# Optimization experiments

Measured on AMD Instinct MI355X. Metric: run time of the kernel, lower is better.

## Reference

```python
import jax, jax.numpy as jnp
import numpy as np

SCALE = 8.0  # sqrt(d_k=64)


def setup_inputs() -> dict:
    key = jax.random.key(0)
    kq, kk, kv, km = jax.random.split(key, 4)
    B, L, D = 8, 4096, 64
    q = jax.random.normal(kq, (B, L, D), dtype=jnp.float32)
    k = jax.random.normal(kk, (B, L, D), dtype=jnp.float32)
    v = jax.random.normal(kv, (B, L, D), dtype=jnp.float32)
    mask = jax.random.randint(km, (B, L, L), 0, 2) == 1  # True = masked out
    return {"q": q, "k": k, "v": v, "mask": mask}


def reference(q, k, v, mask):
    # scores: [B, Lq, Lk]
    u = jnp.einsum('bqd,bkd->bqk', q, k) / SCALE
    u = jnp.where(mask, -jnp.inf, u)
    attn = jax.nn.softmax(u, axis=2)
    output = jnp.einsum('bqk,bkd->bqd', attn, v)
    return (attn, output)
```

## Files before the change

kernel.cpp:

```cpp
#include <hip/hip_runtime.h>
#include <hip/hip_bf16.h>
#include <stdint.h>

#define BB 8
#define LL 4096
#define DD 64
#define KT 64
#define NT (LL / KT)
#define NP2 (LL / 128)

typedef short bf16x8 __attribute__((ext_vector_type(8)));
typedef short bf16x2 __attribute__((ext_vector_type(2)));
typedef float f32x4 __attribute__((ext_vector_type(4)));

#define QSCALE 0.1803368801111204f

__device__ inline short f2bfs(float x) {
    __hip_bfloat16 h = __float2bfloat16(x);
    return __builtin_bit_cast(short, h);
}

__device__ inline bf16x8 pack8v(f32x4 a, f32x4 b) {
    bf16x8 r;
    r[0] = f2bfs(a[0]); r[1] = f2bfs(a[1]); r[2] = f2bfs(a[2]); r[3] = f2bfs(a[3]);
    r[4] = f2bfs(b[0]); r[5] = f2bfs(b[1]); r[6] = f2bfs(b[2]); r[7] = f2bfs(b[3]);
    return r;
}

__device__ inline int swzK(int r) { return (r & 3) | (((r >> 3) & 1) << 2); }
__device__ inline int swzV(int r) { return (r & 7) ^ ((r >> 3) & 7); }

__device__ inline void wg_barrier() {
    asm volatile("s_waitcnt lgkmcnt(0)" ::: "memory");
    __builtin_amdgcn_s_barrier();
    __builtin_amdgcn_sched_barrier(0);
}

__global__ void detect_mask_kernel(const uint32_t* __restrict__ w, uint32_t* __restrict__ flag) {
    __shared__ int nonbin;
    if (threadIdx.x == 0) nonbin = 0;
    __syncthreads();
    int bad = 0;
    for (int i = threadIdx.x; i < 4096; i += 256) bad |= (w[i] > 1u) ? 1 : 0;
    if (bad) atomicOr(&nonbin, 1);
    __syncthreads();
    if (threadIdx.x == 0) *flag = (uint32_t)(nonbin != 0);
}

__global__ __launch_bounds__(512, 4) void fused_attn_kernel(
    const float* __restrict__ qg, const float* __restrict__ kg,
    const float* __restrict__ vg, const void* __restrict__ maskv,
    const uint32_t* __restrict__ flagp,
    float* __restrict__ attn, float* __restrict__ outp)
{
    __shared__ alignas(16) ushort KB[4][KT * 64];
    __shared__ uint8_t Msk[8][NT][64];
    __shared__ float Rs[128];

    const int tid = (int)threadIdx.x;
    const int w   = tid >> 6, l = tid & 63;
    const int lr  = l & 15, lg = l >> 4;
    const int rg  = w & 3, ch = w >> 2;
    const int id  = (int)blockIdx.x;
    const int b   = id & 7;
    const int q0  = (id >> 3) * 64;
    const bool mbyte = (*flagp != 0);

    const float* kb = kg + (size_t)b * LL * DD;
    const float* vb = vg + (size_t)b * LL * DD;

    const int qrow = q0 + 16 * rg + lr;
    const uint8_t* mrow8  = (const uint8_t*)maskv + (size_t)b * LL * LL + (size_t)qrow * LL + ch * 32 + lg * 8;
    const int*     mrow32 = (const int*)maskv     + (size_t)b * LL * LL + (size_t)qrow * LL + ch * 32 + lg * 8;
    float* arow = attn + (size_t)b * LL * LL + (size_t)qrow * LL + ch * 32 + lg * 8;

    bf16x8 qf0, qf1;
    {
        const float* qp = qg + (size_t)(b * LL + qrow) * DD + lg * 8;
        qf0 = pack8v(*(const f32x4*)(qp)      * QSCALE, *(const f32x4*)(qp + 4)  * QSCALE);
        qf1 = pack8v(*(const f32x4*)(qp + 32) * QSCALE, *(const f32x4*)(qp + 36) * QSCALE);
    }

    const int krow0 = tid >> 3, kc8 = tid & 7;
    const int vk2 = tid >> 4, vd4 = tid & 15;

    f32x4 kS0, kS1, vS0, vS1; uint64_t mS = 0;
    auto issS = [&](int kt) {
        const int kbase = kt * KT;
        const float* p = kb + (size_t)(kbase + krow0) * DD + kc8 * 8;
        kS0 = *(const f32x4*)p; kS1 = *(const f32x4*)(p + 4);
        const float* pv = vb + (size_t)(kbase + vk2 * 2) * DD + vd4 * 4;
        vS0 = *(const f32x4*)pv; vS1 = *(const f32x4*)(pv + DD);
        if (mbyte) mS = *(const uint64_t*)(mrow8 + kbase);
    };
    auto comS = [&](int buf) {
        *(bf16x8*)&KB[buf][krow0 * 64 + ((kc8 ^ swzK(krow0)) << 3)] = pack8v(kS0, kS1);
        const int k0 = vk2 * 2;
        #pragma unroll
        for (int e = 0; e < 4; ++e) {
            const int d = vd4 * 4 + e;
            bf16x2 t; t[0] = f2bfs(vS0[e]); t[1] = f2bfs(vS1[e]);
            *(bf16x2*)&KB[2 + buf][d * 64 + (((k0 >> 3) ^ swzV(d)) << 3) + (k0 & 7)] = t;
        }
    };

    float rsum = 0.f;
    f32x4 oacc[4];
    #pragma unroll
    for (int g = 0; g < 4; ++g) { f32x4 z = {0.f, 0.f, 0.f, 0.f}; oacc[g] = z; }

    auto p1body = [&](int buf, uint64_t mu, int kt) {
        const int kbase = kt * KT;
        int4 mi0 = {0,0,0,0}, mi1 = {0,0,0,0};
        if (!mbyte) { mi0 = *(const int4*)(mrow32 + kbase); mi1 = *(const int4*)(mrow32 + kbase + 4); }
        uint32_t mbits = 0;
        float p8[8];
        #pragma unroll
        for (int n = 0; n < 2; ++n) {
            const int krow = ch * 32 + ((lr >> 2) << 3) + (n << 2) + (lr & 3);
            bf16x8 k0 = *(const bf16x8*)&KB[buf][krow * 64 + ((lg       ^ swzK(krow)) << 3)];
            bf16x8 k1 = *(const bf16x8*)&KB[buf][krow * 64 + (((4 + lg) ^ swzK(krow)) << 3)];
            f32x4 c = {0.f, 0.f, 0.f, 0.f};
            c = __builtin_amdgcn_mfma_f32_16x16x32_bf16(k0, qf0, c, 0, 0, 0);
            c = __builtin_amdgcn_mfma_f32_16x16x32_bf16(k1, qf1, c, 0, 0, 0);
            #pragma unroll
            for (int j = 0; j < 4; ++j) {
                const int t = n * 4 + j;
                int mk;
                if (mbyte) mk = (int)((mu >> (8 * t)) & 0xffu);
                else {
                    const int4 mi = n ? mi1 : mi0;
                    mk = (j == 0) ? mi.x : (j == 1) ? mi.y : (j == 2) ? mi.z : mi.w;
                }
                mbits |= (mk ? 1u : 0u) << t;
                const float pv = mk ? 0.f : exp2f(c[j]);
                rsum += pv;
                p8[t] = pv;
            }
        }
        Msk[w][kt][l] = (uint8_t)mbits;
        bf16x8 pa;
        #pragma unroll
        for (int t = 0; t < 8; ++t) pa[t] = f2bfs(p8[t]);
        __builtin_amdgcn_s_setprio(1);
        #pragma unroll
        for (int g = 0; g < 4; ++g) {
            const int d = g * 16 + lr;
            bf16x8 vf = *(const bf16x8*)&KB[2 + buf][d * 64 + (((ch * 4 + lg) ^ swzV(d)) << 3)];
            oacc[g] = __builtin_amdgcn_mfma_f32_16x16x32_bf16(pa, vf, oacc[g], 0, 0, 0);
        }
        __builtin_amdgcn_s_setprio(0);
    };

    issS(0);
    __builtin_amdgcn_sched_barrier(0);
    comS(0);
    wg_barrier();
    #pragma unroll 1
    for (int kt = 0; kt < NT; ++kt) {
        const int cur = kt & 1;
        const bool more = (kt < NT - 1);
        const uint64_t mu = mS;
        if (more) issS(kt + 1);
        __builtin_amdgcn_sched_barrier(0);
        p1body(cur, mu, kt);
        if (more) comS(cur ^ 1);
        wg_barrier();
    }

    rsum += __shfl_xor(rsum, 16, 64);
    rsum += __shfl_xor(rsum, 32, 64);
    if (lg == 0) Rs[ch * 64 + 16 * rg + lr] = rsum;
    __syncthreads();
    const float rinv = 1.0f / (Rs[16 * rg + lr] + Rs[64 + 16 * rg + lr]);

    float* OutL = (float*)KB;
    if (ch == 1) {
        #pragma unroll
        for (int g = 0; g < 4; ++g)
            #pragma unroll
            for (int j = 0; j < 4; ++j)
                OutL[rg * 1088 + (lg * 4 + j) * 68 + g * 16 + lr] = oacc[g][j];
    }
    __syncthreads();
    if (ch == 0) {
        #pragma unroll
        for (int j = 0; j < 4; ++j) {
            const int ql = 16 * rg + lg * 4 + j;
            const float ri = 1.0f / (Rs[ql] + Rs[64 + ql]);
            const size_t orow = (size_t)(b * LL + q0 + ql) * DD;
            #pragma unroll
            for (int g = 0; g < 4; ++g)
                outp[orow + g * 16 + lr] = (oacc[g][j] + OutL[rg * 1088 + (lg * 4 + j) * 68 + g * 16 + lr]) * ri;
        }
    }
    __syncthreads();

    f32x4 k2[4];
    auto iss2 = [&](int kt2) {
        #pragma unroll
        for (int m = 0; m < 2; ++m) {
            const float* p = kb + (size_t)(kt2 * 128 + krow0 + 64 * m) * DD + kc8 * 8;
            k2[2 * m]     = *(const f32x4*)p;
            k2[2 * m + 1] = *(const f32x4*)(p + 4);
        }
    };
    auto com2 = [&](int pair) {
        #pragma unroll
        for (int m = 0; m < 2; ++m)
            *(bf16x8*)&KB[2 * pair + m][krow0 * 64 + ((kc8 ^ swzK(krow0)) << 3)] = pack8v(k2[2 * m], k2[2 * m + 1]);
    };
    auto p2body = [&](int pair, int idx) {
        const int kbase2 = idx * 128;
        #pragma unroll
        for (int h = 0; h < 2; ++h) {
            const int mb2 = (int)Msk[w][2 * idx + h][l];
            const ushort* Kbuf = KB[2 * pair + h];
            #pragma unroll
            for (int n = 0; n < 2; ++n) {
                const int krow = ch * 32 + ((lr >> 2) << 3) + (n << 2) + (lr & 3);
                bf16x8 k0 = *(const bf16x8*)&Kbuf[krow * 64 + ((lg       ^ swzK(krow)) << 3)];
                bf16x8 k1 = *(const bf16x8*)&Kbuf[krow * 64 + (((4 + lg) ^ swzK(krow)) << 3)];
                f32x4 c = {0.f, 0.f, 0.f, 0.f};
                c = __builtin_amdgcn_mfma_f32_16x16x32_bf16(k0, qf0, c, 0, 0, 0);
                c = __builtin_amdgcn_mfma_f32_16x16x32_bf16(k1, qf1, c, 0, 0, 0);
                f32x4 pv;
                #pragma unroll
                for (int j = 0; j < 4; ++j)
                    pv[j] = ((mb2 >> (n * 4 + j)) & 1) ? 0.f : exp2f(c[j]) * rinv;
                *(f32x4*)(arow + kbase2 + h * 64 + n * 4) = pv;
            }
        }
    };

    iss2(0);
    __builtin_amdgcn_sched_barrier(0);
    com2(0);
    wg_barrier();
    #pragma unroll 1
    for (int kt2 = 0; kt2 < NP2; ++kt2) {
        const int pair = kt2 & 1;
        const bool more = (kt2 < NP2 - 1);
        if (more) iss2(kt2 + 1);
        __builtin_amdgcn_sched_barrier(0);
        p2body(pair, kt2);
        if (more) com2(pair ^ 1);
        wg_barrier();
    }
}

extern "C" void kernel_launch(void* const* d_in, const int* in_sizes, int n_in,
                              void* d_out, int out_size, void* d_ws, size_t ws_size,
                              hipStream_t stream) {
    const float* q = (const float*)d_in[0];
    const float* k = (const float*)d_in[1];
    const float* v = (const float*)d_in[2];
    const void* mask = d_in[3];
    float* attn = (float*)d_out;
    float* outp = attn + (size_t)BB * LL * LL;
    uint32_t* flagp = (uint32_t*)d_ws;

    detect_mask_kernel<<<1, 256, 0, stream>>>((const uint32_t*)mask, flagp);
    fused_attn_kernel<<<dim3((LL / 64) * BB), 512, 0, stream>>>(q, k, v, mask, flagp, attn, outp);
}
```

Before: 368.1 us.

## Deepen phase-1 K/V prefetch to two tiles ahead and drop loop-tail branches

Phase 1 now keeps two register staging sets (A/B) and issues global loads for tile kt+2 while computing tile kt. This gives more time to hide memory latency. The loop is unrolled by two and wraps indices modulo the tile count, so the last iterations do redundant but harmless loads and LDS writes instead of branching. Phase 2 likewise drops the 'more' guard and always prefetches with a wrapped index. The cost is more live registers and some wasted loads and stores at the tail.

Result: no change. 362.7 us (-1.5%).

```diff
diff --git a/kernel.cpp b/kernel.cpp
--- a/kernel.cpp
+++ b/kernel.cpp
@@ -84,22 +84,41 @@
     const int krow0 = tid >> 3, kc8 = tid & 7;
     const int vk2 = tid >> 4, vd4 = tid & 15;
 
-    f32x4 kS0, kS1, vS0, vS1; uint64_t mS = 0;
-    auto issS = [&](int kt) {
+    f32x4 kA0, kA1, vA0, vA1; uint64_t mA = 0;
+    f32x4 kB0, kB1, vB0, vB1; uint64_t mB = 0;
+    auto issA = [&](int kt) {
         const int kbase = kt * KT;
         const float* p = kb + (size_t)(kbase + krow0) * DD + kc8 * 8;
-        kS0 = *(const f32x4*)p; kS1 = *(const f32x4*)(p + 4);
+        kA0 = *(const f32x4*)p; kA1 = *(const f32x4*)(p + 4);
         const float* pv = vb + (size_t)(kbase + vk2 * 2) * DD + vd4 * 4;
-        vS0 = *(const f32x4*)pv; vS1 = *(const f32x4*)(pv + DD);
-        if (mbyte) mS = *(const uint64_t*)(mrow8 + kbase);
-    };
-    auto comS = [&](int buf) {
-        *(bf16x8*)&KB[buf][krow0 * 64 + ((kc8 ^ swzK(krow0)) << 3)] = pack8v(kS0, kS1);
+        vA0 = *(const f32x4*)pv; vA1 = *(const f32x4*)(pv + DD);
+        if (mbyte) mA = *(const uint64_t*)(mrow8 + kbase);
+    };
+    auto issB = [&](int kt) {
+        const int kbase = kt * KT;
+        const float* p = kb + (size_t)(kbase + krow0) * DD + kc8 * 8;
+        kB0 = *(const f32x4*)p; kB1 = *(const f32x4*)(p + 4);
+        const float* pv = vb + (size_t)(kbase + vk2 * 2) * DD + vd4 * 4;
+        vB0 = *(const f32x4*)pv; vB1 = *(const f32x4*)(pv + DD);
+        if (mbyte) mB = *(const uint64_t*)(mrow8 + kbase);
+    };
+    auto comA = [&](int buf) {
+        *(bf16x8*)&KB[buf][krow0 * 64 + ((kc8 ^ swzK(krow0)) << 3)] = pack8v(kA0, kA1);
         const int k0 = vk2 * 2;
         #pragma unroll
         for (int e = 0; e < 4; ++e) {
             const int d = vd4 * 4 + e;
-            bf16x2 t; t[0] = f2bfs(vS0[e]); t[1] = f2bfs(vS1[e]);
+            bf16x2 t; t[0] = f2bfs(vA0[e]); t[1] = f2bfs(vA1[e]);
+            *(bf16x2*)&KB[2 + buf][d * 64 + (((k0 >> 3) ^ swzV(d)) << 3) + (k0 & 7)] = t;
+        }
+    };
+    auto comB = [&](int buf) {
+        *(bf16x8*)&KB[buf][krow0 * 64 + ((kc8 ^ swzK(krow0)) << 3)] = pack8v(kB0, kB1);
+        const int k0 = vk2 * 2;
+        #pragma unroll
+        for (int e = 0; e < 4; ++e) {
+            const int d = vd4 * 4 + e;
+            bf16x2 t; t[0] = f2bfs(vB0[e]); t[1] = f2bfs(vB1[e]);
             *(bf16x2*)&KB[2 + buf][d * 64 + (((k0 >> 3) ^ swzV(d)) << 3) + (k0 & 7)] = t;
         }
     };
@@ -152,20 +171,28 @@
         __builtin_amdgcn_s_setprio(0);
     };
 
-    issS(0);
+    issA(0); issB(1);
     __builtin_amdgcn_sched_barrier(0);
-    comS(0);
+    comA(0);
     wg_barrier();
     #pragma unroll 1
-    for (int kt = 0; kt < NT; ++kt) {
-        const int cur = kt & 1;
-        const bool more = (kt < NT - 1);
-        const uint64_t mu = mS;
-        if (more) issS(kt + 1);
-        __builtin_amdgcn_sched_barrier(0);
-        p1body(cur, mu, kt);
-        if (more) comS(cur ^ 1);
-        wg_barrier();
+    for (int kt = 0; kt < NT; kt += 2) {
+        {
+            const uint64_t mu = mA;
+            issA((kt + 2) & (NT - 1));
+            __builtin_amdgcn_sched_barrier(0);
+            p1body(0, mu, kt);
+            comB(1);
+            wg_barrier();
+        }
+        {
+            const uint64_t mu = mB;
+            issB((kt + 3) & (NT - 1));
+            __builtin_amdgcn_sched_barrier(0);
+            p1body(1, mu, kt + 1);
+            comA(0);
+            wg_barrier();
+        }
     }
 
     rsum += __shfl_xor(rsum, 16, 64);
@@ -240,11 +267,10 @@
     #pragma unroll 1
     for (int kt2 = 0; kt2 < NP2; ++kt2) {
         const int pair = kt2 & 1;
-        const bool more = (kt2 < NP2 - 1);
-        if (more) iss2(kt2 + 1);
+        iss2((kt2 + 1) & (NP2 - 1));
         __builtin_amdgcn_sched_barrier(0);
         p2body(pair, kt2);
-        if (more) com2(pair ^ 1);
+        com2(pair ^ 1);
         wg_barrier();
     }
 }
```

## Pre-convert K and transposed V to bf16 and stream tiles via direct-to-LDS loads

Applied to the files above, without the earlier changes.

Adds two prep kernels: one converts K to bf16, the other converts V to a transposed bf16 layout, both written into workspace. The main kernel then fills its swizzled LDS tiles with global_load_lds DMA instead of register loads followed by convert-and-store. Both phases get a two-deep prefetch pipeline controlled by explicit vmcnt waits. This halves the bytes of K/V read per block and removes the VALU conversion work from the hot loop, at the cost of extra launches and hand-tuned waitcnt accounting. Phase 2 also adds int32-mask loads whose results are never used.

New measurement: 352.6 us. 4.2% less time.

```diff
diff --git a/kernel.cpp b/kernel.cpp
--- a/kernel.cpp
+++ b/kernel.cpp
@@ -10,7 +10,6 @@
 #define NP2 (LL / 128)
 
 typedef short bf16x8 __attribute__((ext_vector_type(8)));
-typedef short bf16x2 __attribute__((ext_vector_type(2)));
 typedef float f32x4 __attribute__((ext_vector_type(4)));
 
 #define QSCALE 0.1803368801111204f
@@ -36,6 +35,11 @@
     __builtin_amdgcn_sched_barrier(0);
 }
 
+__device__ inline void gl_lds16(const ushort* g, ushort* l) {
+    __builtin_amdgcn_global_load_lds((const __attribute__((address_space(1))) void*)g,
+                                     (__attribute__((address_space(3))) void*)l, 16, 0, 0);
+}
+
 __global__ void detect_mask_kernel(const uint32_t* __restrict__ w, uint32_t* __restrict__ flag) {
     __shared__ int nonbin;
     if (threadIdx.x == 0) nonbin = 0;
@@ -47,9 +51,36 @@
     if (threadIdx.x == 0) *flag = (uint32_t)(nonbin != 0);
 }
 
+__global__ void convert_k_kernel(const float* __restrict__ src, ushort* __restrict__ dst) {
+    const int i = blockIdx.x * 256 + threadIdx.x;
+    f32x4 a = *(const f32x4*)(src + (size_t)i * 8);
+    f32x4 b = *(const f32x4*)(src + (size_t)i * 8 + 4);
+    *(bf16x8*)(dst + (size_t)i * 8) = pack8v(a, b);
+}
+
+__global__ void convert_vt_kernel(const float* __restrict__ v, ushort* __restrict__ vt) {
+    __shared__ alignas(16) float Lt[64][68];
+    const int kt = blockIdx.x, b = blockIdx.y;
+    const int tid = (int)threadIdx.x;
+    const int r = tid >> 2, c4 = tid & 3;
+    const float* vb = v + ((size_t)b * LL + kt * 64) * DD;
+    #pragma unroll
+    for (int j = 0; j < 4; ++j)
+        *(f32x4*)&Lt[r][c4 * 16 + j * 4] = *(const f32x4*)(vb + (size_t)r * DD + c4 * 16 + j * 4);
+    __syncthreads();
+    ushort* vout = vt + (size_t)b * DD * LL + (size_t)r * LL + kt * 64 + c4 * 16;
+    bf16x8 o0, o1;
+    #pragma unroll
+    for (int j = 0; j < 8; ++j) o0[j] = f2bfs(Lt[c4 * 16 + j][r]);
+    #pragma unroll
+    for (int j = 0; j < 8; ++j) o1[j] = f2bfs(Lt[c4 * 16 + 8 + j][r]);
+    *(bf16x8*)vout = o0;
+    *(bf16x8*)(vout + 8) = o1;
+}
+
 __global__ __launch_bounds__(512, 4) void fused_attn_kernel(
-    const float* __restrict__ qg, const float* __restrict__ kg,
-    const float* __restrict__ vg, const void* __restrict__ maskv,
+    const float* __restrict__ qg, const ushort* __restrict__ kbf,
+    const ushort* __restrict__ vtb, const void* __restrict__ maskv,
     const uint32_t* __restrict__ flagp,
     float* __restrict__ attn, float* __restrict__ outp)
 {
@@ -66,8 +97,8 @@
     const int q0  = (id >> 3) * 64;
     const bool mbyte = (*flagp != 0);
 
-    const float* kb = kg + (size_t)b * LL * DD;
-    const float* vb = vg + (size_t)b * LL * DD;
+    const ushort* kb = kbf + (size_t)b * LL * DD;
+    const ushort* vtg = vtb + (size_t)b * DD * LL;
 
     const int qrow = q0 + 16 * rg + lr;
     const uint8_t* mrow8  = (const uint8_t*)maskv + (size_t)b * LL * LL + (size_t)qrow * LL + ch * 32 + lg * 8;
@@ -81,38 +112,33 @@
         qf1 = pack8v(*(const f32x4*)(qp + 32) * QSCALE, *(const f32x4*)(qp + 36) * QSCALE);
     }
 
-    const int krow0 = tid >> 3, kc8 = tid & 7;
-    const int vk2 = tid >> 4, vd4 = tid & 15;
-
-    f32x4 kS0, kS1, vS0, vS1; uint64_t mS = 0;
-    auto issS = [&](int kt) {
-        const int kbase = kt * KT;
-        const float* p = kb + (size_t)(kbase + krow0) * DD + kc8 * 8;
-        kS0 = *(const f32x4*)p; kS1 = *(const f32x4*)(p + 4);
-        const float* pv = vb + (size_t)(kbase + vk2 * 2) * DD + vd4 * 4;
-        vS0 = *(const f32x4*)pv; vS1 = *(const f32x4*)(pv + DD);
-        if (mbyte) mS = *(const uint64_t*)(mrow8 + kbase);
-    };
-    auto comS = [&](int buf) {
-        *(bf16x8*)&KB[buf][krow0 * 64 + ((kc8 ^ swzK(krow0)) << 3)] = pack8v(kS0, kS1);
-        const int k0 = vk2 * 2;
-        #pragma unroll
-        for (int e = 0; e < 4; ++e) {
-            const int d = vd4 * 4 + e;
-            bf16x2 t; t[0] = f2bfs(vS0[e]); t[1] = f2bfs(vS1[e]);
-            *(bf16x2*)&KB[2 + buf][d * 64 + (((k0 >> 3) ^ swzV(d)) << 3) + (k0 & 7)] = t;
-        }
-    };
+    const int drow = w * 8 + (l >> 3);
+    const int dc   = l & 7;
+    const int kchunk = dc ^ swzK(drow);
+    const int vchunk = dc ^ swzV(drow);
+    ushort* ldsK0 = &KB[0][0] + (tid >> 6) * 512;
+    auto dmaK = [&](int kt, int buf) {
+        gl_lds16(kb + (size_t)(kt * KT + drow) * 64 + 8 * kchunk, &KB[buf][w * 512]);
+    };
+    auto dmaV = [&](int kt, int buf) {
+        gl_lds16(vtg + (size_t)drow * LL + kt * KT + 8 * vchunk, &KB[2 + buf][w * 512]);
+    };
+    auto dmaK2 = [&](int kt2, int pair) {
+        gl_lds16(kb + (size_t)(kt2 * 128 + drow) * 64 + 8 * kchunk, &KB[2 * pair][w * 512]);
+        gl_lds16(kb + (size_t)(kt2 * 128 + 64 + drow) * 64 + 8 * kchunk, &KB[2 * pair + 1][w * 512]);
+    };
+    unsigned long long mA = 0, mB = 0;
+    #define ASM_MLOAD(dst, kt) { unsigned long long a_ = (unsigned long long)(uintptr_t)(mrow8 + (kt) * KT); \
+        asm volatile("global_load_dwordx2 %0, %1, off" : "=v"(dst) : "v"(a_) : "memory"); }
 
     float rsum = 0.f;
     f32x4 oacc[4];
     #pragma unroll
     for (int g = 0; g < 4; ++g) { f32x4 z = {0.f, 0.f, 0.f, 0.f}; oacc[g] = z; }
 
-    auto p1body = [&](int buf, uint64_t mu, int kt) {
-        const int kbase = kt * KT;
+    auto body1 = [&](int buf, unsigned long long mu, int kt) {
         int4 mi0 = {0,0,0,0}, mi1 = {0,0,0,0};
-        if (!mbyte) { mi0 = *(const int4*)(mrow32 + kbase); mi1 = *(const int4*)(mrow32 + kbase + 4); }
+        if (!mbyte) { mi0 = *(const int4*)(mrow32 + kt * KT); mi1 = *(const int4*)(mrow32 + kt * KT + 4); }
         uint32_t mbits = 0;
         float p8[8];
         #pragma unroll
@@ -152,20 +178,24 @@
         __builtin_amdgcn_s_setprio(0);
     };
 
-    issS(0);
-    __builtin_amdgcn_sched_barrier(0);
-    comS(0);
-    wg_barrier();
+    dmaK(0, 0); dmaV(0, 0); if (mbyte) ASM_MLOAD(mA, 0);
+    dmaK(1, 1); dmaV(1, 1); if (mbyte) ASM_MLOAD(mB, 1);
     #pragma unroll 1
-    for (int kt = 0; kt < NT; ++kt) {
-        const int cur = kt & 1;
-        const bool more = (kt < NT - 1);
-        const uint64_t mu = mS;
-        if (more) issS(kt + 1);
+    for (int kt = 0; kt < NT; kt += 2) {
+        if (mbyte) asm volatile("s_waitcnt vmcnt(3)" ::: "memory");
+        else       asm volatile("s_waitcnt vmcnt(2)" ::: "memory");
         __builtin_amdgcn_sched_barrier(0);
-        p1body(cur, mu, kt);
-        if (more) comS(cur ^ 1);
-        wg_barrier();
+        wg_barrier();
+        body1(0, mA, kt);
+        wg_barrier();
+        if (kt + 2 < NT) { dmaK(kt + 2, 0); dmaV(kt + 2, 0); if (mbyte) ASM_MLOAD(mA, kt + 2); }
+        if (mbyte) asm volatile("s_waitcnt vmcnt(3)" ::: "memory");
+        else       asm volatile("s_waitcnt vmcnt(2)" ::: "memory");
+        __builtin_amdgcn_sched_barrier(0);
+        wg_barrier();
+        body1(1, mB, kt + 1);
+        wg_barrier();
+        if (kt + 3 < NT) { dmaK(kt + 3, 1); dmaV(kt + 3, 1); if (mbyte) ASM_MLOAD(mB, kt + 3); }
     }
 
     rsum += __shfl_xor(rsum, 16, 64);
@@ -196,26 +226,18 @@
     }
     __syncthreads();
 
-    f32x4 k2[4];
-    auto iss2 = [&](int kt2) {
-        #pragma unroll
-        for (int m = 0; m < 2; ++m) {
-            const float* p = kb + (size_t)(kt2 * 128 + krow0 + 64 * m) * DD + kc8 * 8;
-            k2[2 * m]     = *(const f32x4*)p;
-            k2[2 * m + 1] = *(const f32x4*)(p + 4);
-        }
-    };
-    auto com2 = [&](int pair) {
-        #pragma unroll
-        for (int m = 0; m < 2; ++m)
-            *(bf16x8*)&KB[2 * pair + m][krow0 * 64 + ((kc8 ^ swzK(krow0)) << 3)] = pack8v(k2[2 * m], k2[2 * m + 1]);
-    };
-    auto p2body = [&](int pair, int idx) {
+    auto body2 = [&](int pair, int idx) {
         const int kbase2 = idx * 128;
         #pragma unroll
         for (int h = 0; h < 2; ++h) {
             const int mb2 = (int)Msk[w][2 * idx + h][l];
             const ushort* Kbuf = KB[2 * pair + h];
+            int4 mi0 = {0,0,0,0}, mi1 = {0,0,0,0};
+            if (!mbyte) {
+                mi0 = *(const int4*)(mrow32 + kbase2 + h * 64);
+                mi1 = *(const int4*)(mrow32 + kbase2 + h * 64 + 4);
+            }
+            (void)mi0; (void)mi1;
             #pragma unroll
             for (int n = 0; n < 2; ++n) {
                 const int krow = ch * 32 + ((lr >> 2) << 3) + (n << 2) + (lr & 3);
@@ -233,19 +255,16 @@
         }
     };
 
-    iss2(0);
-    __builtin_amdgcn_sched_barrier(0);
-    com2(0);
-    wg_barrier();
+    dmaK2(0, 0); dmaK2(1, 1);
     #pragma unroll 1
     for (int kt2 = 0; kt2 < NP2; ++kt2) {
         const int pair = kt2 & 1;
-        const bool more = (kt2 < NP2 - 1);
-        if (more) iss2(kt2 + 1);
+        asm volatile("s_waitcnt vmcnt(2)" ::: "memory");
         __builtin_amdgcn_sched_barrier(0);
-        p2body(pair, kt2);
-        if (more) com2(pair ^ 1);
-        wg_barrier();
+        wg_barrier();
+        body2(pair, kt2);
+        wg_barrier();
+        if (kt2 + 2 < NP2) dmaK2(kt2 + 2, pair);
     }
 }
 
@@ -259,7 +278,11 @@
     float* attn = (float*)d_out;
     float* outp = attn + (size_t)BB * LL * LL;
     uint32_t* flagp = (uint32_t*)d_ws;
+    ushort* kbf = (ushort*)((char*)d_ws + 4096);
+    ushort* vtb = kbf + (size_t)BB * LL * DD;
 
     detect_mask_kernel<<<1, 256, 0, stream>>>((const uint32_t*)mask, flagp);
-    fused_attn_kernel<<<dim3((LL / 64) * BB), 512, 0, stream>>>(q, k, v, mask, flagp, attn, outp);
-}
+    convert_k_kernel<<<dim3(BB * LL * DD / 8 / 256), 256, 0, stream>>>(k, kbf);
+    convert_vt_kernel<<<dim3(LL / 64, BB), 256, 0, stream>>>(v, vtb);
+    fused_attn_kernel<<<dim3((LL / 64) * BB), 512, 0, stream>>>(q, kbf, vtb, mask, flagp, attn, outp);
+}
```
